# Optimization experiments

Measured on AMD Instinct MI355X. Metric: run time of the kernel, lower is better.

Reference implementation:

```python
import jax, jax.numpy as jnp
import numpy as np

NUM_HEADS = 8
N_POINTS = 9
OFFSET_SCALE = 4.0


def bilinear_sample(fmap_flat, xy, H, W):
    """fmap_flat: (BH, H*W, C) row-major spatial; xy: (BH, S, 2) pixel coords (x, y).
    grid_sample(mode='bilinear', padding_mode='zeros', align_corners=True) equivalent.
    Returns (BH, S, C)."""
    x, y = xy[..., 0], xy[..., 1]
    x0 = jnp.floor(x); y0 = jnp.floor(y)
    x1 = x0 + 1.0;    y1 = y0 + 1.0
    wx1 = x - x0; wx0 = 1.0 - wx1
    wy1 = y - y0; wy0 = 1.0 - wy1

    def corner(xi, yi, wgt):
        valid = (xi >= 0) & (xi <= W - 1) & (yi >= 0) & (yi <= H - 1)
        xi_c = jnp.clip(xi, 0, W - 1).astype(jnp.int32)
        yi_c = jnp.clip(yi, 0, H - 1).astype(jnp.int32)
        idx = yi_c * W + xi_c                                   # (BH, S)
        vals = jnp.take_along_axis(fmap_flat, idx[..., None], axis=1)  # (BH, S, C)
        return vals * (wgt * valid.astype(fmap_flat.dtype))[..., None]

    return (corner(x0, y0, wx0 * wy0) + corner(x1, y0, wx1 * wy0)
            + corner(x0, y1, wx0 * wy1) + corner(x1, y1, wx1 * wy1))


def setup_inputs() -> dict:
    key = jax.random.key(0)
    ks = jax.random.split(key, 10)
    B, N, D = 4, 6400, 256
    Hh, P = NUM_HEADS, N_POINTS
    s = 0.02
    return {
        "x":    jax.random.normal(ks[0], (B, N, D), dtype=jnp.float32),
        "Wq":   jax.random.normal(ks[1], (D, D), dtype=jnp.float32) * s,
        "bq":   jnp.zeros((D,), jnp.float32),
        "Woff": jax.random.normal(ks[2], (Hh * P * 2, D), dtype=jnp.float32) * s,
        "boff": jax.random.normal(ks[3], (Hh * P * 2,), dtype=jnp.float32) * s,
        "Wkv":  jax.random.normal(ks[4], (2 * D, D), dtype=jnp.float32) * s,
        "bkv":  jnp.zeros((2 * D,), jnp.float32),
        "Wout": jax.random.normal(ks[5], (D, D), dtype=jnp.float32) * s,
        "bout": jnp.zeros((D,), jnp.float32),
        "h": 40,
        "w": 160,
    }


def reference(x, Wq, bq, Woff, boff, Wkv, bkv, Wout, bout, h, w):
    B, N, D = x.shape
    H, P = NUM_HEADS, N_POINTS
    hd = D // H

    # queries: (B, H, N, hd)
    q = (x @ Wq.T + bq).reshape(B, N, H, hd).transpose(0, 2, 1, 3)

    # per-query per-head offsets in pixels: (B, N, H, P, 2) (dx, dy)
    offsets = jnp.tanh(x @ Woff.T + boff).reshape(B, N, H, P, 2) * OFFSET_SCALE

    # K/V feature maps via 1x1 conv == per-token linear; split heads, flat spatial
    kv = x @ Wkv.T + bkv                     # (B, N, 2D)
    k = kv[..., :D]
    v = kv[..., D:]
    k_flat = k.reshape(B, N, H, hd).transpose(0, 2, 1, 3).reshape(B * H, N, hd)
    v_flat = v.reshape(B, N, H, hd).transpose(0, 2, 1, 3).reshape(B * H, N, hd)

    # base pixel grid (x, y), row-major over (h, w)
    ys, xs = jnp.meshgrid(jnp.arange(h, dtype=x.dtype), jnp.arange(w, dtype=x.dtype), indexing="ij")
    base_xy = jnp.stack([xs, ys], axis=-1).reshape(N, 2)

    # sampling locations: (B, N, H, P, 2) -> (B*H, N*P, 2)
    sample_xy = base_xy[None, :, None, None, :] + offsets
    sample_xy = sample_xy.transpose(0, 2, 1, 3, 4).reshape(B * H, N * P, 2)

    sampled_k = bilinear_sample(k_flat, sample_xy, h, w).reshape(B, H, N, P, hd)
    sampled_v = bilinear_sample(v_flat, sample_xy, h, w).reshape(B, H, N, P, hd)

    logits = jnp.einsum("bhnd,bhnpd->bhnp", q, sampled_k) * (hd ** -0.5)
    attn = jax.nn.softmax(logits, axis=-1)
    out = jnp.einsum("bhnp,bhnpd->bhnd", attn, sampled_v)   # (B, H, N, hd)
    out = out.transpose(0, 2, 1, 3).reshape(B, N, D)
    return out @ Wout.T + bout
```

## Files before the change

### kernel.cpp

```cpp
#include <hip/hip_runtime.h>
#include <math.h>

#define BSZ    4
#define NTOK   6400
#define DMODEL 256
#define NHEAD  8
#define HDIM   32
#define NPTS   9
#define HSP    40
#define WSP    160
#define KDIM   256
#define MTOT   (BSZ*NTOK)

typedef short  short8  __attribute__((ext_vector_type(8)));
typedef float  floatx4 __attribute__((ext_vector_type(4)));

__device__ __forceinline__ ushort f2bf(float f) {
    uint u = __float_as_uint(f);
    u = (u + 0x7FFFu + ((u >> 16) & 1u)) >> 16;
    return (ushort)u;
}

__device__ __forceinline__ void unpack8(uint4 u, float* f) {
    f[0] = __uint_as_float(u.x << 16); f[1] = __uint_as_float(u.x & 0xFFFF0000u);
    f[2] = __uint_as_float(u.y << 16); f[3] = __uint_as_float(u.y & 0xFFFF0000u);
    f[4] = __uint_as_float(u.z << 16); f[5] = __uint_as_float(u.z & 0xFFFF0000u);
    f[6] = __uint_as_float(u.w << 16); f[7] = __uint_as_float(u.w & 0xFFFF0000u);
}

#define AS1C(p) ((const __attribute__((address_space(1))) void*)(p))
#define AS3(p)  ((__attribute__((address_space(3))) void*)(p))

__global__ __launch_bounds__(256) void cast_all(
    const float* __restrict__ x,   const float* __restrict__ Wq,
    const float* __restrict__ Woff,const float* __restrict__ Wkv,
    const float* __restrict__ Wout,
    ushort* __restrict__ xb, ushort* __restrict__ wqb, ushort* __restrict__ woffb,
    ushort* __restrict__ wkvb, ushort* __restrict__ woutb)
{
    const int bid = blockIdx.x;
    const float* src; ushort* dst; int base;
    if      (bid < 6400) { src = x;    dst = xb;    base = bid; }
    else if (bid < 6464) { src = Wq;   dst = wqb;   base = bid - 6400; }
    else if (bid < 6500) { src = Woff; dst = woffb; base = bid - 6464; }
    else if (bid < 6628) { src = Wkv;  dst = wkvb;  base = bid - 6500; }
    else                 { src = Wout; dst = woutb; base = bid - 6628; }
    const int i = base * 1024 + threadIdx.x * 4;
    float4 v = *(const float4*)(src + i);
    ushort4 o;
    o.x = f2bf(v.x); o.y = f2bf(v.y); o.z = f2bf(v.z); o.w = f2bf(v.w);
    *(ushort4*)(dst + i) = o;
}

template <int MODE>
__global__ __launch_bounds__(256) void gemm_bf16(
    const ushort* __restrict__ Xb,
    const ushort* __restrict__ Wb,
    const float* __restrict__ bias,
    void* __restrict__ Yv, void* __restrict__ Y2v,
    int Ncols)
{
    __shared__ ushort As[128 * 32];
    __shared__ ushort Bs[128 * 32];

    const int tid = threadIdx.x;
    const int block_m = blockIdx.y * 128;
    const int block_n = blockIdx.x * 128;
    const int wave = tid >> 6, lane = tid & 63;
    const int wm = (wave >> 1) * 64, wn = (wave & 1) * 64;
    const int l15 = lane & 15, quad = lane >> 4;

    const int srow = wave * 32 + (lane >> 2);
    const int scol = (lane & 3) * 8;

    const ushort* gA0 = Xb + (size_t)(block_m + srow) * KDIM + scol;
    const ushort* gA1 = gA0 + 16 * KDIM;
    int bc0 = block_n + srow, bc1 = bc0 + 16;
    if (MODE == 1) { bc0 = min(bc0, Ncols - 1); bc1 = min(bc1, Ncols - 1); }
    const ushort* gB0 = Wb + (size_t)bc0 * KDIM + scol;
    const ushort* gB1 = Wb + (size_t)bc1 * KDIM + scol;

    ushort* lA0 = &As[(wave * 32) * 32];
    ushort* lA1 = &As[(wave * 32 + 16) * 32];
    ushort* lB0 = &Bs[(wave * 32) * 32];
    ushort* lB1 = &Bs[(wave * 32 + 16) * 32];

    floatx4 acc[4][4];
    #pragma unroll
    for (int i = 0; i < 4; ++i)
        #pragma unroll
        for (int j = 0; j < 4; ++j) {
            acc[i][j][0] = 0.f; acc[i][j][1] = 0.f;
            acc[i][j][2] = 0.f; acc[i][j][3] = 0.f;
        }

    for (int k0 = 0; k0 < KDIM; k0 += 32) {
        __builtin_amdgcn_global_load_lds(AS1C(gA0 + k0), AS3(lA0), 16, 0, 0);
        __builtin_amdgcn_global_load_lds(AS1C(gA1 + k0), AS3(lA1), 16, 0, 0);
        __builtin_amdgcn_global_load_lds(AS1C(gB0 + k0), AS3(lB0), 16, 0, 0);
        __builtin_amdgcn_global_load_lds(AS1C(gB1 + k0), AS3(lB1), 16, 0, 0);
        __syncthreads();

        short8 af[4], bfr[4];
        #pragma unroll
        for (int f = 0; f < 4; ++f) {
            af[f]  = *(const short8*)&As[(wm + f * 16 + l15) * 32 + quad * 8];
            bfr[f] = *(const short8*)&Bs[(wn + f * 16 + l15) * 32 + quad * 8];
        }
        #pragma unroll
        for (int fm = 0; fm < 4; ++fm)
            #pragma unroll
            for (int fn = 0; fn < 4; ++fn)
                acc[fm][fn] = __builtin_amdgcn_mfma_f32_16x16x32_bf16(
                    af[fm], bfr[fn], acc[fm][fn], 0, 0, 0);
        __syncthreads();
    }

    #pragma unroll
    for (int fn = 0; fn < 4; ++fn) {
        const int col = block_n + wn + fn * 16 + l15;
        const float bcol = (MODE == 1 && col >= Ncols) ? 0.f : bias[col];
        #pragma unroll
        for (int fm = 0; fm < 4; ++fm) {
            #pragma unroll
            for (int r = 0; r < 4; ++r) {
                const int row = block_m + wm + fm * 16 + quad * 4 + r;
                const float val = acc[fm][fn][r] + bcol;
                if (MODE == 0) {
                    ((ushort*)Yv)[(size_t)row * DMODEL + col] = f2bf(val);
                } else if (MODE == 1) {
                    if (col < Ncols)
                        ((float*)Yv)[(size_t)row * 144 + col] = tanhf(val) * 4.0f;
                } else if (MODE == 2) {
                    const int b = row / NTOK, n = row % NTOK;
                    const int hh = (col & 255) >> 5, c = col & 31;
                    const size_t o = (((size_t)(b * NHEAD + hh)) * NTOK + n) * HDIM + c;
                    if (col < DMODEL) ((ushort*)Yv)[o]  = f2bf(val);
                    else              ((ushort*)Y2v)[o] = f2bf(val);
                } else {
                    ((float*)Yv)[(size_t)row * DMODEL + col] = val;
                }
            }
        }
    }
}

__global__ __launch_bounds__(256) void deform_attn(
    const ushort* __restrict__ qb,
    const float* __restrict__ off,
    const ushort* __restrict__ kfb,
    const ushort* __restrict__ vfb,
    ushort* __restrict__ attnb)
{
    const int lane = threadIdx.x & 63;
    const int token = blockIdx.x * 8 + (threadIdx.x >> 6) * 2 + (lane >> 5);
    const int h = (lane >> 2) & 7, lc = lane & 3;
    const int b = token / NTOK, n = token % NTOK;

    const uint4 qu = *(const uint4*)(qb + (size_t)token * DMODEL + h * HDIM + lc * 8);
    float q[8]; unpack8(qu, q);

    const float* ob = off + (size_t)token * 144 + h * (NPTS * 2);
    float2 offs[NPTS];
    #pragma unroll
    for (int p = 0; p < NPTS; ++p) offs[p] = *(const float2*)(ob + 2 * p);

    const float bx = (float)(n % WSP), by = (float)(n / WSP);
    const ushort* kb = kfb + (size_t)(b * NHEAD + h) * NTOK * HDIM + lc * 8;
    const ushort* vb = vfb + (size_t)(b * NHEAD + h) * NTOK * HDIM + lc * 8;

    float m = -INFINITY, s = 0.f;
    float o[8];
    #pragma unroll
    for (int c = 0; c < 8; ++c) o[c] = 0.f;

    #pragma unroll
    for (int p = 0; p < NPTS; ++p) {
        const float sx = bx + offs[p].x, sy = by + offs[p].y;
        const float fx0 = floorf(sx), fy0 = floorf(sy);
        const float wx1 = sx - fx0, wx0 = 1.0f - wx1;
        const float wy1 = sy - fy0, wy0 = 1.0f - wy1;
        const int ix0 = (int)fx0, iy0 = (int)fy0;
        const int ix1 = ix0 + 1, iy1 = iy0 + 1;
        const bool vx0 = (ix0 >= 0) & (ix0 <= WSP - 1);
        const bool vx1 = (ix1 >= 0) & (ix1 <= WSP - 1);
        const bool vy0 = (iy0 >= 0) & (iy0 <= HSP - 1);
        const bool vy1 = (iy1 >= 0) & (iy1 <= HSP - 1);
        const int cx0 = min(max(ix0, 0), WSP - 1);
        const int cx1 = min(max(ix1, 0), WSP - 1);
        const int cy0 = min(max(iy0, 0), HSP - 1);
        const int cy1 = min(max(iy1, 0), HSP - 1);
        const float w00 = wx0 * wy0 * (float)(vx0 && vy0);
        const float w10 = wx1 * wy0 * (float)(vx1 && vy0);
        const float w01 = wx0 * wy1 * (float)(vx0 && vy1);
        const float w11 = wx1 * wy1 * (float)(vx1 && vy1);
        const int i00 = (cy0 * WSP + cx0) * HDIM;
        const int i10 = (cy0 * WSP + cx1) * HDIM;
        const int i01 = (cy1 * WSP + cx0) * HDIM;
        const int i11 = (cy1 * WSP + cx1) * HDIM;

        const uint4 ku0 = *(const uint4*)(kb + i00);
        const uint4 ku1 = *(const uint4*)(kb + i10);
        const uint4 ku2 = *(const uint4*)(kb + i01);
        const uint4 ku3 = *(const uint4*)(kb + i11);
        const uint4 vu0 = *(const uint4*)(vb + i00);
        const uint4 vu1 = *(const uint4*)(vb + i10);
        const uint4 vu2 = *(const uint4*)(vb + i01);
        const uint4 vu3 = *(const uint4*)(vb + i11);

        float kc[8], d00 = 0.f, d10 = 0.f, d01 = 0.f, d11 = 0.f;
        unpack8(ku0, kc);
        #pragma unroll
        for (int c = 0; c < 8; ++c) d00 = fmaf(q[c], kc[c], d00);
        unpack8(ku1, kc);
        #pragma unroll
        for (int c = 0; c < 8; ++c) d10 = fmaf(q[c], kc[c], d10);
        unpack8(ku2, kc);
        #pragma unroll
        for (int c = 0; c < 8; ++c) d01 = fmaf(q[c], kc[c], d01);
        unpack8(ku3, kc);
        #pragma unroll
        for (int c = 0; c < 8; ++c) d11 = fmaf(q[c], kc[c], d11);

        float part = w00 * d00 + w10 * d10 + w01 * d01 + w11 * d11;
        part += __shfl_xor(part, 1, 64);
        part += __shfl_xor(part, 2, 64);
        const float l = part * 0.17677669529663687f;

        const float m1 = fmaxf(m, l);
        const float corr = __expf(m - m1);
        const float e = __expf(l - m1);
        s = fmaf(s, corr, e);
        m = m1;

        const float e00 = e * w00, e10 = e * w10, e01 = e * w01, e11 = e * w11;
        float v0[8], v1[8], v2[8], v3[8];
        unpack8(vu0, v0); unpack8(vu1, v1); unpack8(vu2, v2); unpack8(vu3, v3);
        #pragma unroll
        for (int c = 0; c < 8; ++c)
            o[c] = fmaf(o[c], corr,
                        fmaf(e00, v0[c], fmaf(e10, v1[c], fmaf(e01, v2[c], e11 * v3[c]))));
    }

    const float inv = 1.0f / s;
    uint4 ru;
    ru.x = (uint)f2bf(o[0] * inv) | ((uint)f2bf(o[1] * inv) << 16);
    ru.y = (uint)f2bf(o[2] * inv) | ((uint)f2bf(o[3] * inv) << 16);
    ru.z = (uint)f2bf(o[4] * inv) | ((uint)f2bf(o[5] * inv) << 16);
    ru.w = (uint)f2bf(o[6] * inv) | ((uint)f2bf(o[7] * inv) << 16);
    *(uint4*)(attnb + (size_t)token * DMODEL + h * HDIM + lc * 8) = ru;
}

extern "C" void kernel_launch(void* const* d_in, const int* in_sizes, int n_in,
                              void* d_out, int out_size, void* d_ws, size_t ws_size,
                              hipStream_t stream) {
    const float* x    = (const float*)d_in[0];
    const float* Wq   = (const float*)d_in[1];
    const float* bq   = (const float*)d_in[2];
    const float* Woff = (const float*)d_in[3];
    const float* boff = (const float*)d_in[4];
    const float* Wkv  = (const float*)d_in[5];
    const float* bkv  = (const float*)d_in[6];
    const float* Wout = (const float*)d_in[7];
    const float* bout = (const float*)d_in[8];

    ushort* xb    = (ushort*)d_ws;
    ushort* qb    = xb + (size_t)MTOT * DMODEL;
    float*  off   = (float*)(qb + (size_t)MTOT * DMODEL);
    ushort* kfb   = (ushort*)(off + (size_t)MTOT * 144);
    ushort* vfb   = kfb + (size_t)MTOT * DMODEL;
    ushort* wqb   = vfb + (size_t)MTOT * DMODEL;
    ushort* woffb = wqb + 65536;
    ushort* wkvb  = woffb + 36864;
    ushort* woutb = wkvb + 131072;
    ushort* attnb = xb;

    cast_all<<<dim3(6692), dim3(256), 0, stream>>>(x, Wq, Woff, Wkv, Wout,
                                                   xb, wqb, woffb, wkvb, woutb);

    gemm_bf16<0><<<dim3(2, 200), dim3(256), 0, stream>>>(xb, wqb, bq, qb, nullptr, 256);
    gemm_bf16<1><<<dim3(2, 200), dim3(256), 0, stream>>>(xb, woffb, boff, off, nullptr, 144);
    gemm_bf16<2><<<dim3(4, 200), dim3(256), 0, stream>>>(xb, wkvb, bkv, kfb, vfb, 512);
    deform_attn<<<dim3(3200), dim3(256), 0, stream>>>(qb, off, kfb, vfb, attnb);
    gemm_bf16<3><<<dim3(2, 200), dim3(256), 0, stream>>>(attnb, woutb, bout, d_out, nullptr, 256);
}
```

Measured before the change: 216.0 us.

## Fuse Q/offset/KV projections into one GEMM and batch deform-attn points

Concatenates the Wq, Woff (zero-padded to 256 rows) and Wkv weights into one 1024-row bf16 matrix so a single GEMM launch produces q, offsets, K and V, replacing three launches that each reread x. The deform_attn kernel now processes sampling points in groups of three, issuing the K gathers for a group together, doing one online-softmax rescale per group, and using packed float2 vector math for the dot products and V accumulation. It also adds a dedicated output GEMM kernel. The padding adds some wasted MFMA work on zero weight rows, and the grouped loop may raise register pressure.

```diff
diff --git a/kernel.cpp b/kernel.cpp
--- a/kernel.cpp
+++ b/kernel.cpp
@@ -14,6 +14,7 @@
 
 typedef short  short8  __attribute__((ext_vector_type(8)));
 typedef float  floatx4 __attribute__((ext_vector_type(4)));
+typedef float  f32x2   __attribute__((ext_vector_type(2)));
 
 __device__ __forceinline__ ushort f2bf(float f) {
     uint u = __float_as_uint(f);
@@ -21,11 +22,25 @@
     return (ushort)u;
 }
 
-__device__ __forceinline__ void unpack8(uint4 u, float* f) {
-    f[0] = __uint_as_float(u.x << 16); f[1] = __uint_as_float(u.x & 0xFFFF0000u);
-    f[2] = __uint_as_float(u.y << 16); f[3] = __uint_as_float(u.y & 0xFFFF0000u);
-    f[4] = __uint_as_float(u.z << 16); f[5] = __uint_as_float(u.z & 0xFFFF0000u);
-    f[6] = __uint_as_float(u.w << 16); f[7] = __uint_as_float(u.w & 0xFFFF0000u);
+__device__ __forceinline__ void unpack8v(uint4 u, f32x2* f) {
+    f[0].x = __uint_as_float(u.x << 16); f[0].y = __uint_as_float(u.x & 0xFFFF0000u);
+    f[1].x = __uint_as_float(u.y << 16); f[1].y = __uint_as_float(u.y & 0xFFFF0000u);
+    f[2].x = __uint_as_float(u.z << 16); f[2].y = __uint_as_float(u.z & 0xFFFF0000u);
+    f[3].x = __uint_as_float(u.w << 16); f[3].y = __uint_as_float(u.w & 0xFFFF0000u);
+}
+
+__device__ __forceinline__ float dot8(uint4 u, const f32x2* q2) {
+    f32x2 a; a.x = 0.f; a.y = 0.f;
+    f32x2 t;
+    t.x = __uint_as_float(u.x << 16); t.y = __uint_as_float(u.x & 0xFFFF0000u);
+    a += t * q2[0];
+    t.x = __uint_as_float(u.y << 16); t.y = __uint_as_float(u.y & 0xFFFF0000u);
+    a += t * q2[1];
+    t.x = __uint_as_float(u.z << 16); t.y = __uint_as_float(u.z & 0xFFFF0000u);
+    a += t * q2[2];
+    t.x = __uint_as_float(u.w << 16); t.y = __uint_as_float(u.w & 0xFFFF0000u);
+    a += t * q2[3];
+    return a.x + a.y;
 }
 
 #define AS1C(p) ((const __attribute__((address_space(1))) void*)(p))
@@ -35,16 +50,21 @@
     const float* __restrict__ x,   const float* __restrict__ Wq,
     const float* __restrict__ Woff,const float* __restrict__ Wkv,
     const float* __restrict__ Wout,
-    ushort* __restrict__ xb, ushort* __restrict__ wqb, ushort* __restrict__ woffb,
-    ushort* __restrict__ wkvb, ushort* __restrict__ woutb)
+    ushort* __restrict__ xb, ushort* __restrict__ wf, ushort* __restrict__ woutb)
 {
     const int bid = blockIdx.x;
+    if (bid >= 6500 && bid < 6528) {
+        const int i = (bid - 6500) * 1024 + threadIdx.x * 4;
+        ushort4 z; z.x = 0; z.y = 0; z.z = 0; z.w = 0;
+        *(ushort4*)(wf + 400 * 256 + i) = z;
+        return;
+    }
     const float* src; ushort* dst; int base;
-    if      (bid < 6400) { src = x;    dst = xb;    base = bid; }
-    else if (bid < 6464) { src = Wq;   dst = wqb;   base = bid - 6400; }
-    else if (bid < 6500) { src = Woff; dst = woffb; base = bid - 6464; }
-    else if (bid < 6628) { src = Wkv;  dst = wkvb;  base = bid - 6500; }
-    else                 { src = Wout; dst = woutb; base = bid - 6628; }
+    if      (bid < 6400) { src = x;    dst = xb;              base = bid; }
+    else if (bid < 6464) { src = Wq;   dst = wf;              base = bid - 6400; }
+    else if (bid < 6500) { src = Woff; dst = wf + 256 * 256;  base = bid - 6464; }
+    else if (bid < 6656) { src = Wkv;  dst = wf + 512 * 256;  base = bid - 6528; }
+    else                 { src = Wout; dst = woutb;           base = bid - 6656; }
     const int i = base * 1024 + threadIdx.x * 4;
     float4 v = *(const float4*)(src + i);
     ushort4 o;
@@ -52,13 +72,13 @@
     *(ushort4*)(dst + i) = o;
 }
 
-template <int MODE>
-__global__ __launch_bounds__(256) void gemm_bf16(
+__global__ __launch_bounds__(256) void gemm_fused(
     const ushort* __restrict__ Xb,
-    const ushort* __restrict__ Wb,
-    const float* __restrict__ bias,
-    void* __restrict__ Yv, void* __restrict__ Y2v,
-    int Ncols)
+    const ushort* __restrict__ Wf,
+    const float* __restrict__ bq, const float* __restrict__ boff,
+    const float* __restrict__ bkv,
+    ushort* __restrict__ qb, float* __restrict__ off,
+    ushort* __restrict__ kfb, ushort* __restrict__ vfb)
 {
     __shared__ ushort As[128 * 32];
     __shared__ ushort Bs[128 * 32];
@@ -75,10 +95,8 @@
 
     const ushort* gA0 = Xb + (size_t)(block_m + srow) * KDIM + scol;
     const ushort* gA1 = gA0 + 16 * KDIM;
-    int bc0 = block_n + srow, bc1 = bc0 + 16;
-    if (MODE == 1) { bc0 = min(bc0, Ncols - 1); bc1 = min(bc1, Ncols - 1); }
-    const ushort* gB0 = Wb + (size_t)bc0 * KDIM + scol;
-    const ushort* gB1 = Wb + (size_t)bc1 * KDIM + scol;
+    const ushort* gB0 = Wf + (size_t)(block_n + srow) * KDIM + scol;
+    const ushort* gB1 = gB0 + 16 * KDIM;
 
     ushort* lA0 = &As[(wave * 32) * 32];
     ushort* lA1 = &As[(wave * 32 + 16) * 32];
@@ -119,27 +137,104 @@
     #pragma unroll
     for (int fn = 0; fn < 4; ++fn) {
         const int col = block_n + wn + fn * 16 + l15;
-        const float bcol = (MODE == 1 && col >= Ncols) ? 0.f : bias[col];
+        float bcol;
+        if      (col < 256) bcol = bq[col];
+        else if (col < 400) bcol = boff[col - 256];
+        else if (col < 512) bcol = 0.f;
+        else                bcol = bkv[col - 512];
         #pragma unroll
         for (int fm = 0; fm < 4; ++fm) {
             #pragma unroll
             for (int r = 0; r < 4; ++r) {
                 const int row = block_m + wm + fm * 16 + quad * 4 + r;
                 const float val = acc[fm][fn][r] + bcol;
-                if (MODE == 0) {
-                    ((ushort*)Yv)[(size_t)row * DMODEL + col] = f2bf(val);
-                } else if (MODE == 1) {
-                    if (col < Ncols)
-                        ((float*)Yv)[(size_t)row * 144 + col] = tanhf(val) * 4.0f;
-                } else if (MODE == 2) {
-                    const int b = row / NTOK, n = row % NTOK;
-                    const int hh = (col & 255) >> 5, c = col & 31;
-                    const size_t o = (((size_t)(b * NHEAD + hh)) * NTOK + n) * HDIM + c;
-                    if (col < DMODEL) ((ushort*)Yv)[o]  = f2bf(val);
-                    else              ((ushort*)Y2v)[o] = f2bf(val);
-                } else {
-                    ((float*)Yv)[(size_t)row * DMODEL + col] = val;
+                if (col < 256) {
+                    qb[(size_t)row * DMODEL + col] = f2bf(val);
+                } else if (col < 400) {
+                    off[(size_t)row * 144 + (col - 256)] = tanhf(val) * 4.0f;
+                } else if (col >= 512) {
+                    const int c2 = col - 512;
+                    const int bb = row / NTOK, nn = row % NTOK;
+                    const int hh = (c2 & 255) >> 5, cc = c2 & 31;
+                    const size_t o = (((size_t)(bb * NHEAD + hh)) * NTOK + nn) * HDIM + cc;
+                    if (c2 < 256) kfb[o] = f2bf(val);
+                    else          vfb[o] = f2bf(val);
                 }
+            }
+        }
+    }
+}
+
+__global__ __launch_bounds__(256) void gemm_out(
+    const ushort* __restrict__ Xb,
+    const ushort* __restrict__ Wb,
+    const float* __restrict__ bias,
+    float* __restrict__ Y)
+{
+    __shared__ ushort As[128 * 32];
+    __shared__ ushort Bs[128 * 32];
+
+    const int tid = threadIdx.x;
+    const int block_m = blockIdx.y * 128;
+    const int block_n = blockIdx.x * 128;
+    const int wave = tid >> 6, lane = tid & 63;
+    const int wm = (wave >> 1) * 64, wn = (wave & 1) * 64;
+    const int l15 = lane & 15, quad = lane >> 4;
+
+    const int srow = wave * 32 + (lane >> 2);
+    const int scol = (lane & 3) * 8;
+
+    const ushort* gA0 = Xb + (size_t)(block_m + srow) * KDIM + scol;
+    const ushort* gA1 = gA0 + 16 * KDIM;
+    const ushort* gB0 = Wb + (size_t)(block_n + srow) * KDIM + scol;
+    const ushort* gB1 = gB0 + 16 * KDIM;
+
+    ushort* lA0 = &As[(wave * 32) * 32];
+    ushort* lA1 = &As[(wave * 32 + 16) * 32];
+    ushort* lB0 = &Bs[(wave * 32) * 32];
+    ushort* lB1 = &Bs[(wave * 32 + 16) * 32];
+
+    floatx4 acc[4][4];
+    #pragma unroll
+    for (int i = 0; i < 4; ++i)
+        #pragma unroll
+        for (int j = 0; j < 4; ++j) {
+            acc[i][j][0] = 0.f; acc[i][j][1] = 0.f;
+            acc[i][j][2] = 0.f; acc[i][j][3] = 0.f;
+        }
+
+    for (int k0 = 0; k0 < KDIM; k0 += 32) {
+        __builtin_amdgcn_global_load_lds(AS1C(gA0 + k0), AS3(lA0), 16, 0, 0);
+        __builtin_amdgcn_global_load_lds(AS1C(gA1 + k0), AS3(lA1), 16, 0, 0);
+        __builtin_amdgcn_global_load_lds(AS1C(gB0 + k0), AS3(lB0), 16, 0, 0);
+        __builtin_amdgcn_global_load_lds(AS1C(gB1 + k0), AS3(lB1), 16, 0, 0);
+        __syncthreads();
+
+        short8 af[4], bfr[4];
+        #pragma unroll
+        for (int f = 0; f < 4; ++f) {
+            af[f]  = *(const short8*)&As[(wm + f * 16 + l15) * 32 + quad * 8];
+            bfr[f] = *(const short8*)&Bs[(wn + f * 16 + l15) * 32 + quad * 8];
+        }
+        #pragma unroll
+        for (int fm = 0; fm < 4; ++fm)
+            #pragma unroll
+            for (int fn = 0; fn < 4; ++fn)
+                acc[fm][fn] = __builtin_amdgcn_mfma_f32_16x16x32_bf16(
+                    af[fm], bfr[fn], acc[fm][fn], 0, 0, 0);
+        __syncthreads();
+    }
+
+    #pragma unroll
+    for (int fn = 0; fn < 4; ++fn) {
+        const int col = block_n + wn + fn * 16 + l15;
+        const float bcol = bias[col];
+        #pragma unroll
+        for (int fm = 0; fm < 4; ++fm) {
+            #pragma unroll
+            for (int r = 0; r < 4; ++r) {
+                const int row = block_m + wm + fm * 16 + quad * 4 + r;
+                Y[(size_t)row * DMODEL + col] = acc[fm][fn][r] + bcol;
             }
         }
     }
@@ -158,96 +253,95 @@
     const int b = token / NTOK, n = token % NTOK;
 
     const uint4 qu = *(const uint4*)(qb + (size_t)token * DMODEL + h * HDIM + lc * 8);
-    float q[8]; unpack8(qu, q);
+    f32x2 q2[4]; unpack8v(qu, q2);
 
     const float* ob = off + (size_t)token * 144 + h * (NPTS * 2);
-    float2 offs[NPTS];
-    #pragma unroll
-    for (int p = 0; p < NPTS; ++p) offs[p] = *(const float2*)(ob + 2 * p);
-
     const float bx = (float)(n % WSP), by = (float)(n / WSP);
-    const ushort* kb = kfb + (size_t)(b * NHEAD + h) * NTOK * HDIM + lc * 8;
-    const ushort* vb = vfb + (size_t)(b * NHEAD + h) * NTOK * HDIM + lc * 8;
+    const ushort* kbase = kfb + (size_t)(b * NHEAD + h) * NTOK * HDIM + lc * 8;
+    const ushort* vbase = vfb + (size_t)(b * NHEAD + h) * NTOK * HDIM + lc * 8;
 
     float m = -INFINITY, s = 0.f;
-    float o[8];
-    #pragma unroll
-    for (int c = 0; c < 8; ++c) o[c] = 0.f;
-
-    #pragma unroll
-    for (int p = 0; p < NPTS; ++p) {
-        const float sx = bx + offs[p].x, sy = by + offs[p].y;
-        const float fx0 = floorf(sx), fy0 = floorf(sy);
-        const float wx1 = sx - fx0, wx0 = 1.0f - wx1;
-        const float wy1 = sy - fy0, wy0 = 1.0f - wy1;
-        const int ix0 = (int)fx0, iy0 = (int)fy0;
-        const int ix1 = ix0 + 1, iy1 = iy0 + 1;
-        const bool vx0 = (ix0 >= 0) & (ix0 <= WSP - 1);
-        const bool vx1 = (ix1 >= 0) & (ix1 <= WSP - 1);
-        const bool vy0 = (iy0 >= 0) & (iy0 <= HSP - 1);
-        const bool vy1 = (iy1 >= 0) & (iy1 <= HSP - 1);
-        const int cx0 = min(max(ix0, 0), WSP - 1);
-        const int cx1 = min(max(ix1, 0), WSP - 1);
-        const int cy0 = min(max(iy0, 0), HSP - 1);
-        const int cy1 = min(max(iy1, 0), HSP - 1);
-        const float w00 = wx0 * wy0 * (float)(vx0 && vy0);
-        const float w10 = wx1 * wy0 * (float)(vx1 && vy0);
-        const float w01 = wx0 * wy1 * (float)(vx0 && vy1);
-        const float w11 = wx1 * wy1 * (float)(vx1 && vy1);
-        const int i00 = (cy0 * WSP + cx0) * HDIM;
-        const int i10 = (cy0 * WSP + cx1) * HDIM;
-        const int i01 = (cy1 * WSP + cx0) * HDIM;
-        const int i11 = (cy1 * WSP + cx1) * HDIM;
-
-        const uint4 ku0 = *(const uint4*)(kb + i00);
-        const uint4 ku1 = *(const uint4*)(kb + i10);
-        const uint4 ku2 = *(const uint4*)(kb + i01);
-        const uint4 ku3 = *(const uint4*)(kb + i11);
-        const uint4 vu0 = *(const uint4*)(vb + i00);
-        const uint4 vu1 = *(const uint4*)(vb + i10);
-        const uint4 vu2 = *(const uint4*)(vb + i01);
-        const uint4 vu3 = *(const uint4*)(vb + i11);
-
-        float kc[8], d00 = 0.f, d10 = 0.f, d01 = 0.f, d11 = 0.f;
-        unpack8(ku0, kc);
-        #pragma unroll
-        for (int c = 0; c < 8; ++c) d00 = fmaf(q[c], kc[c], d00);
-        unpack8(ku1, kc);
-        #pragma unroll
-        for (int c = 0; c < 8; ++c) d10 = fmaf(q[c], kc[c], d10);
-        unpack8(ku2, kc);
-        #pragma unroll
-        for (int c = 0; c < 8; ++c) d01 = fmaf(q[c], kc[c], d01);
-        unpack8(ku3, kc);
-        #pragma unroll
-        for (int c = 0; c < 8; ++c) d11 = fmaf(q[c], kc[c], d11);
-
-        float part = w00 * d00 + w10 * d10 + w01 * d01 + w11 * d11;
-        part += __shfl_xor(part, 1, 64);
-        part += __shfl_xor(part, 2, 64);
-        const float l = part * 0.17677669529663687f;
-
-        const float m1 = fmaxf(m, l);
+    f32x2 o2[4];
+    #pragma unroll
+    for (int i = 0; i < 4; ++i) { o2[i].x = 0.f; o2[i].y = 0.f; }
+
+    #pragma unroll
+    for (int g = 0; g < 3; ++g) {
+        int   idx[3][4];
+        float wt[3][4];
+        #pragma unroll
+        for (int j = 0; j < 3; ++j) {
+            const int p = g * 3 + j;
+            const float2 of = *(const float2*)(ob + 2 * p);
+            const float sx = bx + of.x, sy = by + of.y;
+            const float fx0 = floorf(sx), fy0 = floorf(sy);
+            const float wx1 = sx - fx0, wx0 = 1.0f - wx1;
+            const float wy1 = sy - fy0, wy0 = 1.0f - wy1;
+            const int ix0 = (int)fx0, iy0 = (int)fy0;
+            const int ix1 = ix0 + 1, iy1 = iy0 + 1;
+            const bool vx0 = (ix0 >= 0) & (ix0 <= WSP - 1);
+            const bool vx1 = (ix1 >= 0) & (ix1 <= WSP - 1);
+            const bool vy0 = (iy0 >= 0) & (iy0 <= HSP - 1);
+            const bool vy1 = (iy1 >= 0) & (iy1 <= HSP - 1);
+            const int cx0 = min(max(ix0, 0), WSP - 1);
+            const int cx1 = min(max(ix1, 0), WSP - 1);
+            const int cy0 = min(max(iy0, 0), HSP - 1);
+            const int cy1 = min(max(iy1, 0), HSP - 1);
+            wt[j][0] = wx0 * wy0 * (float)(vx0 && vy0);
+            wt[j][1] = wx1 * wy0 * (float)(vx1 && vy0);
+            wt[j][2] = wx0 * wy1 * (float)(vx0 && vy1);
+            wt[j][3] = wx1 * wy1 * (float)(vx1 && vy1);
+            idx[j][0] = (cy0 * WSP + cx0) * HDIM;
+            idx[j][1] = (cy0 * WSP + cx1) * HDIM;
+            idx[j][2] = (cy1 * WSP + cx0) * HDIM;
+            idx[j][3] = (cy1 * WSP + cx1) * HDIM;
+        }
+
+        float l[3];
+        #pragma unroll
+        for (int j = 0; j < 3; ++j) {
+            const uint4 k0 = *(const uint4*)(kbase + idx[j][0]);
+            const uint4 k1 = *(const uint4*)(kbase + idx[j][1]);
+            const uint4 k2 = *(const uint4*)(kbase + idx[j][2]);
+            const uint4 k3 = *(const uint4*)(kbase + idx[j][3]);
+            float part = wt[j][0] * dot8(k0, q2) + wt[j][1] * dot8(k1, q2)
+                       + wt[j][2] * dot8(k2, q2) + wt[j][3] * dot8(k3, q2);
+            part += __shfl_xor(part, 1, 64);
+            part += __shfl_xor(part, 2, 64);
+            l[j] = part * 0.17677669529663687f;
+        }
+
+        const float m1 = fmaxf(fmaxf(fmaxf(l[0], l[1]), l[2]), m);
         const float corr = __expf(m - m1);
-        const float e = __expf(l - m1);
-        s = fmaf(s, corr, e);
+        const float e0 = __expf(l[0] - m1);
+        const float e1 = __expf(l[1] - m1);
+        const float e2 = __expf(l[2] - m1);
+        s = s * corr + e0 + e1 + e2;
         m = m1;
-
-        const float e00 = e * w00, e10 = e * w10, e01 = e * w01, e11 = e * w11;
-        float v0[8], v1[8], v2[8], v3[8];
-        unpack8(vu0, v0); unpack8(vu1, v1); unpack8(vu2, v2); unpack8(vu3, v3);
-        #pragma unroll
-        for (int c = 0; c < 8; ++c)
-            o[c] = fmaf(o[c], corr,
-                        fmaf(e00, v0[c], fmaf(e10, v1[c], fmaf(e01, v2[c], e11 * v3[c]))));
+        const float e[3] = {e0, e1, e2};
+
+        #pragma unroll
+        for (int i = 0; i < 4; ++i) o2[i] *= corr;
+
+        #pragma unroll
+        for (int j = 0; j < 3; ++j) {
+            #pragma unroll
+            for (int c = 0; c < 4; ++c) {
+                const uint4 vu = *(const uint4*)(vbase + idx[j][c]);
+                f32x2 vv[4]; unpack8v(vu, vv);
+                const float ew = e[j] * wt[j][c];
+                #pragma unroll
+                for (int i = 0; i < 4; ++i) o2[i] += vv[i] * ew;
+            }
+        }
     }
 
     const float inv = 1.0f / s;
     uint4 ru;
-    ru.x = (uint)f2bf(o[0] * inv) | ((uint)f2bf(o[1] * inv) << 16);
-    ru.y = (uint)f2bf(o[2] * inv) | ((uint)f2bf(o[3] * inv) << 16);
-    ru.z = (uint)f2bf(o[4] * inv) | ((uint)f2bf(o[5] * inv) << 16);
-    ru.w = (uint)f2bf(o[6] * inv) | ((uint)f2bf(o[7] * inv) << 16);
+    ru.x = (uint)f2bf(o2[0].x * inv) | ((uint)f2bf(o2[0].y * inv) << 16);
+    ru.y = (uint)f2bf(o2[1].x * inv) | ((uint)f2bf(o2[1].y * inv) << 16);
+    ru.z = (uint)f2bf(o2[2].x * inv) | ((uint)f2bf(o2[2].y * inv) << 16);
+    ru.w = (uint)f2bf(o2[3].x * inv) | ((uint)f2bf(o2[3].y * inv) << 16);
     *(uint4*)(attnb + (size_t)token * DMODEL + h * HDIM + lc * 8) = ru;
 }
 
@@ -269,18 +363,18 @@
     float*  off   = (float*)(qb + (size_t)MTOT * DMODEL);
     ushort* kfb   = (ushort*)(off + (size_t)MTOT * 144);
     ushort* vfb   = kfb + (size_t)MTOT * DMODEL;
-    ushort* wqb   = vfb + (size_t)MTOT * DMODEL;
-    ushort* woffb = wqb + 65536;
-    ushort* wkvb  = woffb + 36864;
-    ushort* woutb = wkvb + 131072;
+    ushort* wf    = vfb + (size_t)MTOT * DMODEL;
+    ushort* woutb = wf + 262144;
     ushort* attnb = xb;
 
-    cast_all<<<dim3(6692), dim3(256), 0, stream>>>(x, Wq, Woff, Wkv, Wout,
-                                                   xb, wqb, woffb, wkvb, woutb);
-
-    gemm_bf16<0><<<dim3(2, 200), dim3(256), 0, stream>>>(xb, wqb, bq, qb, nullptr, 256);
-    gemm_bf16<1><<<dim3(2, 200), dim3(256), 0, stream>>>(xb, woffb, boff, off, nullptr, 144);
-    gemm_bf16<2><<<dim3(4, 200), dim3(256), 0, stream>>>(xb, wkvb, bkv, kfb, vfb, 512);
+    cast_all<<<dim3(6720), dim3(256), 0, stream>>>(x, Wq, Woff, Wkv, Wout,
+                                                   xb, wf, woutb);
+
+    gemm_fused<<<dim3(8, 200), dim3(256), 0, stream>>>(xb, wf, bq, boff, bkv,
+                                                       qb, off, kfb, vfb);
+
     deform_attn<<<dim3(3200), dim3(256), 0, stream>>>(qb, off, kfb, vfb, attnb);
-    gemm_bf16<3><<<dim3(2, 200), dim3(256), 0, stream>>>(attnb, woutb, bout, d_out, nullptr, 256);
-}
+
+    gemm_out<<<dim3(2, 200), dim3(256), 0, stream>>>(attnb, woutb, bout,
+                                                     (float*)d_out);
+}
```

Result: no change. 217.4 us (+0.7%).
